# Performance work log

Measured on AMD Instinct MI355X. Metric: run time of the kernel, lower is better.

The kernel has to match this reference:

```python
import jax, jax.numpy as jnp
import numpy as np

H = 64  # GRU hidden size
EPS = 1e-6

def setup_inputs() -> dict:
    key = jax.random.key(0)
    ks = jax.random.split(key, 11)
    B, T = 1_000_000, 12
    return {
        "y_tm1": jax.random.normal(ks[0], (B, 2), jnp.float32),
        "z":     jax.random.normal(ks[1], (B, H), jnp.float32),
        "x":     jax.random.normal(ks[2], (B, T, 2), jnp.float32),  # base-dist sample, sigma=1.0
        "Wih":   jax.random.normal(ks[3], (3 * H, 2), jnp.float32) * 0.1,
        "Whh":   jax.random.normal(ks[4], (3 * H, H), jnp.float32) * 0.1,
        "bih":   jax.random.normal(ks[5], (3 * H,), jnp.float32) * 0.1,
        "bhh":   jax.random.normal(ks[6], (3 * H,), jnp.float32) * 0.1,
        "W1":    jax.random.normal(ks[7], (32, H), jnp.float32) * 0.1,
        "b1":    jax.random.normal(ks[8], (32,), jnp.float32) * 0.1,
        "W2":    jax.random.normal(ks[9], (4, 32), jnp.float32) * 0.1,
        "b2":    jax.random.normal(ks[10], (4,), jnp.float32) * 0.1,
    }

def _gru_cell(inp, h, Wih, Whh, bih, bhh):
    # torch.nn.GRUCell semantics; gates ordered (r, z, n)
    gi = inp @ Wih.T + bih              # [B, 3H]
    gh = h @ Whh.T + bhh                # [B, 3H]
    i_r, i_z, i_n = jnp.split(gi, 3, axis=-1)
    h_r, h_z, h_n = jnp.split(gh, 3, axis=-1)
    r = jax.nn.sigmoid(i_r + h_r)
    u = jax.nn.sigmoid(i_z + h_z)
    n = jnp.tanh(i_n + r * h_n)
    return (1.0 - u) * n + u * h

def reference(y_tm1, z, x, Wih, Whh, bih, bhh, W1, b1, W2, b2):
    def step(carry, x_t):
        y_prev, h = carry
        h = _gru_cell(y_prev, h, Wih, Whh, bih, bhh)
        dls = jax.nn.relu(h @ W1.T + b1) @ W2.T + b2   # [B, 4]
        dloc = dls[:, :2]
        scale = jax.nn.softplus(dls[:, 2:]) + EPS
        y_t = y_prev + dloc + scale * x_t
        return (y_t, h), y_t

    xs = jnp.swapaxes(x, 0, 1)                          # [T, B, 2]
    _, ys = jax.lax.scan(step, (y_tm1, z), xs)
    return jnp.swapaxes(ys, 0, 1)                       # [B, T, 2]
```

## Files before the change

kernel.cpp:

```cpp
#include <hip/hip_runtime.h>
#include <math.h>
#include <stdint.h>


typedef short bf16x8 __attribute__((ext_vector_type(8)));
typedef float f32x4  __attribute__((ext_vector_type(4)));

#define OFF_RZN 0
#define OFF_KS2 12288
#define OFF_W2F 14336
#define OFF_W1P 14848
#define WS_TOT  17152

#define W1LDW 72
#define HLW   104
#define XYW   28

__device__ __forceinline__ short f2bf(float f) {
    union { float f; uint32_t u; } v; v.f = f;
    uint32_t r = v.u + 0x7fffu + ((v.u >> 16) & 1u);
    return (short)(r >> 16);
}
__device__ __forceinline__ uint32_t cvtpk(float lo, float hi) {
    uint32_t r;
    asm("v_cvt_pk_bf16_f32 %0, %1, %2" : "=v"(r) : "v"(lo), "v"(hi));
    return r;
}
__device__ __forceinline__ float sigf(float x) {
    return __builtin_amdgcn_rcpf(1.f + __expf(-x));
}
__device__ __forceinline__ float tanhf1(float x) {
    return 1.f - 2.f * __builtin_amdgcn_rcpf(__expf(2.f * x) + 1.f);
}
__device__ __forceinline__ float softplusf(float x) {
    return fmaxf(x, 0.f) + __logf(1.f + __expf(-fabsf(x)));
}

__global__ void prep_kernel(const float* __restrict__ Wih, const float* __restrict__ Whh,
                            const float* __restrict__ bih, const float* __restrict__ bhh,
                            const float* __restrict__ W1, const float* __restrict__ W2,
                            short* __restrict__ wsw) {
    int idx = blockIdx.x * blockDim.x + threadIdx.x;
    if (idx >= WS_TOT) return;
    float v = 0.f;
    if (idx < OFF_KS2) {
        v = Whh[idx];
    } else if (idx < OFF_W2F) {
        int i = idx - OFF_KS2;
        int s = i >> 9, r = (i >> 3) & 63, j = i & 7;
        if (s == 0) {
            if (j == 0) v = Wih[2 * r];
            else if (j == 1) v = Wih[2 * r + 1];
            else if (j == 2) v = bih[r] + bhh[r];
        } else if (s == 1) {
            int row = 64 + r;
            if (j == 0) v = Wih[2 * row];
            else if (j == 1) v = Wih[2 * row + 1];
            else if (j == 2) v = bih[row] + bhh[row];
        } else if (s == 2) {
            if (j == 2) v = bhh[128 + r];
        } else {
            int row = 128 + r;
            if (j == 0) v = Wih[2 * row];
            else if (j == 1) v = Wih[2 * row + 1];
            else if (j == 2) v = bih[row];
        }
    } else if (idx < OFF_W1P) {
        int i = idx - OFF_W2F;
        int l = i >> 3, j = i & 7;
        int lnn = l & 15, gg = l >> 4;
        v = (lnn < 4) ? W2[lnn * 32 + gg * 8 + j] : 0.f;
    } else {
        int i = idx - OFF_W1P;
        int r = i / W1LDW, c = i - r * W1LDW;
        v = (c < 64) ? W1[r * 64 + c] : 0.f;
    }
    wsw[idx] = f2bf(v);
}

__global__ __launch_bounds__(256, 2)
void arflow4(const float* __restrict__ y_tm1,
             const float* __restrict__ z,
             const float* __restrict__ x,
             const float* __restrict__ b1,
             const float* __restrict__ b2,
             const short* __restrict__ wsw,
             float* __restrict__ out,
             int B, int T)
{
    __shared__ __align__(16) float XY[128 * XYW];
    __shared__ __align__(16) short HL[4][32 * HLW];
    __shared__ __align__(16) short KS2[4 * 64 * 8];
    __shared__ __align__(16) short W1L[32 * W1LDW];

    const int tid  = threadIdx.x;
    const int wave = tid >> 6;
    const int lane = tid & 63;
    const int g    = lane >> 4;
    const int ln   = lane & 15;
    const int base = blockIdx.x * 128;
    const int rows = (B - base < 128) ? (B - base) : 128;
    const int NF4  = T >> 1;
    const bool g0  = (g == 0);

    {
        const float4* xg = reinterpret_cast<const float4*>(x) + (size_t)base * NF4;
        const int tot = 128 * NF4;
        for (int i = tid; i < tot; i += 256) {
            float4 v = (i < rows * NF4) ? xg[i] : make_float4(0.f, 0.f, 0.f, 0.f);
            int r = i / NF4, c = i - r * NF4;
            *reinterpret_cast<float4*>(&XY[r * XYW + c * 4]) = v;
        }
    }
    {
        const uint32_t* src = reinterpret_cast<const uint32_t*>(wsw + OFF_KS2);
        uint32_t* dst = reinterpret_cast<uint32_t*>(KS2);
        for (int i = tid; i < 1024; i += 256) dst[i] = src[i];
        const uint32_t* s1 = reinterpret_cast<const uint32_t*>(wsw + OFF_W1P);
        uint32_t* d1 = reinterpret_cast<uint32_t*>(W1L);
        for (int i = tid; i < (32 * W1LDW) / 2; i += 256) d1[i] = s1[i];
    }

    bf16x8 wR[4][2], wZ[4][2], wN[4][2];
#pragma unroll
    for (int mg = 0; mg < 4; ++mg)
#pragma unroll
        for (int ks = 0; ks < 2; ++ks) {
            wR[mg][ks] = *reinterpret_cast<const bf16x8*>(wsw + ((      mg * 16 + ln) * 64 + ks * 32 + g * 8));
            wZ[mg][ks] = *reinterpret_cast<const bf16x8*>(wsw + ((64  + mg * 16 + ln) * 64 + ks * 32 + g * 8));
            wN[mg][ks] = *reinterpret_cast<const bf16x8*>(wsw + ((128 + mg * 16 + ln) * 64 + ks * 32 + g * 8));
        }
    bf16x8 w2f = *reinterpret_cast<const bf16x8*>(wsw + OFF_W2F + lane * 8);

    f32x4 b1q[2];
#pragma unroll
    for (int mt = 0; mt < 2; ++mt) {
        float4 tv = reinterpret_cast<const float4*>(b1)[mt * 4 + g];
        b1q[mt][0] = tv.x; b1q[mt][1] = tv.y; b1q[mt][2] = tv.z; b1q[mt][3] = tv.w;
    }
    f32x4 dInit;
    {
        float4 bb = *reinterpret_cast<const float4*>(b2);
        dInit[0] = g0 ? bb.x : 0.f;
        dInit[1] = g0 ? bb.y : 0.f;
        dInit[2] = g0 ? bb.z : 0.f;
        dInit[3] = g0 ? bb.w : 0.f;
    }
    const f32x4 Z0 = {0.f, 0.f, 0.f, 0.f};

    float hpr[4][2][4];
    float2 y[2];
    short* hl = &HL[wave][0];
#pragma unroll
    for (int n = 0; n < 2; ++n) {
        int gr = base + wave * 32 + n * 16 + ln;
        bool ok = gr < B;
#pragma unroll
        for (int mg = 0; mg < 4; ++mg) {
            float4 zv = ok ? reinterpret_cast<const float4*>(z)[(size_t)gr * 16 + mg * 4 + g]
                           : make_float4(0.f, 0.f, 0.f, 0.f);
            hpr[mg][n][0] = zv.x; hpr[mg][n][1] = zv.y;
            hpr[mg][n][2] = zv.z; hpr[mg][n][3] = zv.w;
        }
        float2 yv = ok ? reinterpret_cast<const float2*>(y_tm1)[gr] : make_float2(0.f, 0.f);
        y[n] = yv;
    }
#pragma unroll
    for (int n = 0; n < 2; ++n)
#pragma unroll
        for (int mg = 0; mg < 4; ++mg) {
            uint2 pk;
            pk.x = cvtpk(hpr[mg][n][0], hpr[mg][n][1]);
            pk.y = cvtpk(hpr[mg][n][2], hpr[mg][n][3]);
            *reinterpret_cast<uint2*>(&hl[(n * 16 + ln) * HLW + mg * 16 + g * 4]) = pk;
        }
    bf16x8 hb[2][2];
#pragma unroll
    for (int n = 0; n < 2; ++n)
#pragma unroll
        for (int ks = 0; ks < 2; ++ks)
            hb[n][ks] = *reinterpret_cast<const bf16x8*>(&hl[(n * 16 + ln) * HLW + ks * 32 + g * 8]);

    __syncthreads();

    const uint32_t onepk = g0 ? 0x00003F80u : 0u;
    const volatile bf16x8* k2p = reinterpret_cast<const volatile bf16x8*>(&KS2[ln * 8]);
    const volatile bf16x8* w1p = reinterpret_cast<const volatile bf16x8*>(&W1L[ln * W1LDW + g * 8]);

    for (int t = 0; t < T; ++t) {
        bf16x8 yb[2];
#pragma unroll
        for (int n = 0; n < 2; ++n) {
            uint32_t ypk = cvtpk(y[n].x, y[n].y);
            union { bf16x8 v; uint32_t u[4]; } yu;
            yu.u[0] = g0 ? ypk : 0u;
            yu.u[1] = onepk;
            yu.u[2] = 0u; yu.u[3] = 0u;
            yb[n] = yu.v;
        }

#pragma unroll
        for (int mg = 0; mg < 4; ++mg) {
            bf16x8 k2R = k2p[0 * 64 + mg * 16 + 0];
            bf16x8 k2Z = k2p[1 * 64 + mg * 16 + 0];
            bf16x8 k2N = k2p[2 * 64 + mg * 16 + 0];
            bf16x8 k2I = k2p[3 * 64 + mg * 16 + 0];
#pragma unroll
            for (int n = 0; n < 2; ++n) {
                f32x4 aR = __builtin_amdgcn_mfma_f32_16x16x32_bf16(wR[mg][0], hb[n][0], Z0, 0, 0, 0);
                f32x4 aZ = __builtin_amdgcn_mfma_f32_16x16x32_bf16(wZ[mg][0], hb[n][0], Z0, 0, 0, 0);
                f32x4 aN = __builtin_amdgcn_mfma_f32_16x16x32_bf16(wN[mg][0], hb[n][0], Z0, 0, 0, 0);
                f32x4 aI = __builtin_amdgcn_mfma_f32_16x16x32_bf16(k2I,       yb[n],    Z0, 0, 0, 0);
                aR = __builtin_amdgcn_mfma_f32_16x16x32_bf16(wR[mg][1], hb[n][1], aR, 0, 0, 0);
                aZ = __builtin_amdgcn_mfma_f32_16x16x32_bf16(wZ[mg][1], hb[n][1], aZ, 0, 0, 0);
                aN = __builtin_amdgcn_mfma_f32_16x16x32_bf16(wN[mg][1], hb[n][1], aN, 0, 0, 0);
                aR = __builtin_amdgcn_mfma_f32_16x16x32_bf16(k2R, yb[n], aR, 0, 0, 0);
                aZ = __builtin_amdgcn_mfma_f32_16x16x32_bf16(k2Z, yb[n], aZ, 0, 0, 0);
                aN = __builtin_amdgcn_mfma_f32_16x16x32_bf16(k2N, yb[n], aN, 0, 0, 0);

                float hq[4];
#pragma unroll
                for (int q = 0; q < 4; ++q) {
                    float r  = sigf(aR[q]);
                    float u  = sigf(aZ[q]);
                    float nn = tanhf1(fmaf(r, aN[q], aI[q]));
                    float hv = fmaf(u, hpr[mg][n][q] - nn, nn);
                    hpr[mg][n][q] = hv;
                    hq[q] = hv;
                }
                uint2 pk;
                pk.x = cvtpk(hq[0], hq[1]);
                pk.y = cvtpk(hq[2], hq[3]);
                *reinterpret_cast<uint2*>(&hl[(n * 16 + ln) * HLW + mg * 16 + g * 4]) = pk;
            }
        }

#pragma unroll
        for (int n = 0; n < 2; ++n)
#pragma unroll
            for (int ks = 0; ks < 2; ++ks)
                hb[n][ks] = *reinterpret_cast<const bf16x8*>(&hl[(n * 16 + ln) * HLW + ks * 32 + g * 8]);

        f32x4 aM[2][2];
#pragma unroll
        for (int mt = 0; mt < 2; ++mt) {
            bf16x8 wM0 = w1p[mt * 16 * (W1LDW / 8) + 0];
            bf16x8 wM1 = w1p[mt * 16 * (W1LDW / 8) + 4];
#pragma unroll
            for (int n = 0; n < 2; ++n) {
                f32x4 a = __builtin_amdgcn_mfma_f32_16x16x32_bf16(wM0, hb[n][0], b1q[mt], 0, 0, 0);
                aM[mt][n] = __builtin_amdgcn_mfma_f32_16x16x32_bf16(wM1, hb[n][1], a, 0, 0, 0);
            }
        }

#pragma unroll
        for (int n = 0; n < 2; ++n)
#pragma unroll
            for (int mt = 0; mt < 2; ++mt) {
                uint2 pk;
                pk.x = cvtpk(fmaxf(aM[mt][n][0], 0.f), fmaxf(aM[mt][n][1], 0.f));
                pk.y = cvtpk(fmaxf(aM[mt][n][2], 0.f), fmaxf(aM[mt][n][3], 0.f));
                *reinterpret_cast<uint2*>(&hl[(n * 16 + ln) * HLW + 64 + mt * 16 + g * 4]) = pk;
            }
        f32x4 aD[2];
#pragma unroll
        for (int n = 0; n < 2; ++n) {
            bf16x8 ab = *reinterpret_cast<const bf16x8*>(&hl[(n * 16 + ln) * HLW + 64 + g * 8]);
            aD[n] = __builtin_amdgcn_mfma_f32_16x16x32_bf16(w2f, ab, dInit, 0, 0, 0);
        }

#pragma unroll
        for (int n = 0; n < 2; ++n) {
            int rl = wave * 32 + n * 16 + ln;
            float2 xt = *reinterpret_cast<const float2*>(&XY[rl * XYW + t * 2]);
            float s0 = softplusf(aD[n][2]) + 1e-6f;
            float s1 = softplusf(aD[n][3]) + 1e-6f;
            y[n].x += aD[n][0] + s0 * xt.x;
            y[n].y += aD[n][1] + s1 * xt.y;
            if (g0)
                *reinterpret_cast<float2*>(&XY[rl * XYW + t * 2]) = y[n];
        }
    }

    __syncthreads();
    {
        float4* og = reinterpret_cast<float4*>(out) + (size_t)base * NF4;
        const int tot = 128 * NF4;
        for (int i = tid; i < tot; i += 256) {
            if (i < rows * NF4) {
                int r = i / NF4, c = i - r * NF4;
                og[i] = *reinterpret_cast<const float4*>(&XY[r * XYW + c * 4]);
            }
        }
    }
}

extern "C" void kernel_launch(void* const* d_in, const int* in_sizes, int n_in,
                              void* d_out, int out_size, void* d_ws, size_t ws_size,
                              hipStream_t stream) {
    const float* y_tm1 = (const float*)d_in[0];
    const float* z     = (const float*)d_in[1];
    const float* x     = (const float*)d_in[2];
    const float* Wih   = (const float*)d_in[3];
    const float* Whh   = (const float*)d_in[4];
    const float* bih   = (const float*)d_in[5];
    const float* bhh   = (const float*)d_in[6];
    const float* W1    = (const float*)d_in[7];
    const float* b1    = (const float*)d_in[8];
    const float* W2    = (const float*)d_in[9];
    const float* b2    = (const float*)d_in[10];
    float* out = (float*)d_out;
    short* wsw = (short*)d_ws;

    const int B = in_sizes[0] / 2;
    const int T = in_sizes[2] / in_sizes[0];

    hipLaunchKernelGGL(prep_kernel, dim3((WS_TOT + 255) / 256), dim3(256), 0, stream,
                       Wih, Whh, bih, bhh, W1, W2, wsw);

    const int nblk = (B + 127) / 128;
    hipLaunchKernelGGL(arflow4, dim3(nblk), dim3(256), 0, stream,
                       y_tm1, z, x, b1, b2, wsw, out, B, T);
}
```

Measured before the change: 908.3 us.

## Stream Whh fragments from global per step, fold exp scales into weights, raise occupancy

```diff
diff --git a/kernel.cpp b/kernel.cpp
--- a/kernel.cpp
+++ b/kernel.cpp
@@ -16,6 +16,9 @@
 #define HLW   104
 #define XYW   28
 
+#define SCL_RZ (-1.4426950408889634f)
+#define SCL_NI ( 2.8853900817779268f)
+
 __device__ __forceinline__ short f2bf(float f) {
     union { float f; uint32_t u; } v; v.f = f;
     uint32_t r = v.u + 0x7fffu + ((v.u >> 16) & 1u);
@@ -26,12 +29,7 @@
     asm("v_cvt_pk_bf16_f32 %0, %1, %2" : "=v"(r) : "v"(lo), "v"(hi));
     return r;
 }
-__device__ __forceinline__ float sigf(float x) {
-    return __builtin_amdgcn_rcpf(1.f + __expf(-x));
-}
-__device__ __forceinline__ float tanhf1(float x) {
-    return 1.f - 2.f * __builtin_amdgcn_rcpf(__expf(2.f * x) + 1.f);
-}
+__device__ __forceinline__ float rcpf(float x) { return __builtin_amdgcn_rcpf(x); }
 __device__ __forceinline__ float softplusf(float x) {
     return fmaxf(x, 0.f) + __logf(1.f + __expf(-fabsf(x)));
 }
@@ -44,10 +42,13 @@
     if (idx >= WS_TOT) return;
     float v = 0.f;
     if (idx < OFF_KS2) {
-        v = Whh[idx];
+        int row = idx >> 6;
+        float s = (row < 128) ? SCL_RZ : SCL_NI;
+        v = Whh[idx] * s;
     } else if (idx < OFF_W2F) {
         int i = idx - OFF_KS2;
         int s = i >> 9, r = (i >> 3) & 63, j = i & 7;
+        float sc = (s < 2) ? SCL_RZ : SCL_NI;
         if (s == 0) {
             if (j == 0) v = Wih[2 * r];
             else if (j == 1) v = Wih[2 * r + 1];
@@ -65,6 +66,7 @@
             else if (j == 1) v = Wih[2 * row + 1];
             else if (j == 2) v = bih[row];
         }
+        v *= sc;
     } else if (idx < OFF_W1P) {
         int i = idx - OFF_W2F;
         int l = i >> 3, j = i & 7;
@@ -78,8 +80,8 @@
     wsw[idx] = f2bf(v);
 }
 
-__global__ __launch_bounds__(256, 2)
-void arflow4(const float* __restrict__ y_tm1,
+__global__ __launch_bounds__(256, 3)
+void arflow5(const float* __restrict__ y_tm1,
              const float* __restrict__ z,
              const float* __restrict__ x,
              const float* __restrict__ b1,
@@ -121,15 +123,6 @@
         for (int i = tid; i < (32 * W1LDW) / 2; i += 256) d1[i] = s1[i];
     }
 
-    bf16x8 wR[4][2], wZ[4][2], wN[4][2];
-#pragma unroll
-    for (int mg = 0; mg < 4; ++mg)
-#pragma unroll
-        for (int ks = 0; ks < 2; ++ks) {
-            wR[mg][ks] = *reinterpret_cast<const bf16x8*>(wsw + ((      mg * 16 + ln) * 64 + ks * 32 + g * 8));
-            wZ[mg][ks] = *reinterpret_cast<const bf16x8*>(wsw + ((64  + mg * 16 + ln) * 64 + ks * 32 + g * 8));
-            wN[mg][ks] = *reinterpret_cast<const bf16x8*>(wsw + ((128 + mg * 16 + ln) * 64 + ks * 32 + g * 8));
-        }
     bf16x8 w2f = *reinterpret_cast<const bf16x8*>(wsw + OFF_W2F + lane * 8);
 
     f32x4 b1q[2];
@@ -138,14 +131,7 @@
         float4 tv = reinterpret_cast<const float4*>(b1)[mt * 4 + g];
         b1q[mt][0] = tv.x; b1q[mt][1] = tv.y; b1q[mt][2] = tv.z; b1q[mt][3] = tv.w;
     }
-    f32x4 dInit;
-    {
-        float4 bb = *reinterpret_cast<const float4*>(b2);
-        dInit[0] = g0 ? bb.x : 0.f;
-        dInit[1] = g0 ? bb.y : 0.f;
-        dInit[2] = g0 ? bb.z : 0.f;
-        dInit[3] = g0 ? bb.w : 0.f;
-    }
+    const float b20 = b2[0], b21 = b2[1], b22 = b2[2], b23 = b2[3];
     const f32x4 Z0 = {0.f, 0.f, 0.f, 0.f};
 
     float hpr[4][2][4];
@@ -187,7 +173,12 @@
     const volatile bf16x8* k2p = reinterpret_cast<const volatile bf16x8*>(&KS2[ln * 8]);
     const volatile bf16x8* w1p = reinterpret_cast<const volatile bf16x8*>(&W1L[ln * W1LDW + g * 8]);
 
+    const short* wp = wsw;
+    const int woff = ln * 8 + g;
+
     for (int t = 0; t < T; ++t) {
+        asm volatile("" : "+s"(wp));
+
         bf16x8 yb[2];
 #pragma unroll
         for (int n = 0; n < 2; ++n) {
@@ -201,19 +192,27 @@
 
 #pragma unroll
         for (int mg = 0; mg < 4; ++mg) {
-            bf16x8 k2R = k2p[0 * 64 + mg * 16 + 0];
-            bf16x8 k2Z = k2p[1 * 64 + mg * 16 + 0];
-            bf16x8 k2N = k2p[2 * 64 + mg * 16 + 0];
-            bf16x8 k2I = k2p[3 * 64 + mg * 16 + 0];
+            asm volatile("" : "+s"(wp));
+            const bf16x8* wq = reinterpret_cast<const bf16x8*>(wp) + woff;
+            bf16x8 wR0 = wq[(0 * 64 + mg * 16) * 8 + 0];
+            bf16x8 wR1 = wq[(0 * 64 + mg * 16) * 8 + 4];
+            bf16x8 wZ0 = wq[(1 * 64 + mg * 16) * 8 + 0];
+            bf16x8 wZ1 = wq[(1 * 64 + mg * 16) * 8 + 4];
+            bf16x8 wN0 = wq[(2 * 64 + mg * 16) * 8 + 0];
+            bf16x8 wN1 = wq[(2 * 64 + mg * 16) * 8 + 4];
+            bf16x8 k2R = k2p[0 * 64 + mg * 16];
+            bf16x8 k2Z = k2p[1 * 64 + mg * 16];
+            bf16x8 k2N = k2p[2 * 64 + mg * 16];
+            bf16x8 k2I = k2p[3 * 64 + mg * 16];
 #pragma unroll
             for (int n = 0; n < 2; ++n) {
-                f32x4 aR = __builtin_amdgcn_mfma_f32_16x16x32_bf16(wR[mg][0], hb[n][0], Z0, 0, 0, 0);
-                f32x4 aZ = __builtin_amdgcn_mfma_f32_16x16x32_bf16(wZ[mg][0], hb[n][0], Z0, 0, 0, 0);
-                f32x4 aN = __builtin_amdgcn_mfma_f32_16x16x32_bf16(wN[mg][0], hb[n][0], Z0, 0, 0, 0);
-                f32x4 aI = __builtin_amdgcn_mfma_f32_16x16x32_bf16(k2I,       yb[n],    Z0, 0, 0, 0);
-                aR = __builtin_amdgcn_mfma_f32_16x16x32_bf16(wR[mg][1], hb[n][1], aR, 0, 0, 0);
-                aZ = __builtin_amdgcn_mfma_f32_16x16x32_bf16(wZ[mg][1], hb[n][1], aZ, 0, 0, 0);
-                aN = __builtin_amdgcn_mfma_f32_16x16x32_bf16(wN[mg][1], hb[n][1], aN, 0, 0, 0);
+                f32x4 aR = __builtin_amdgcn_mfma_f32_16x16x32_bf16(wR0, hb[n][0], Z0, 0, 0, 0);
+                f32x4 aZ = __builtin_amdgcn_mfma_f32_16x16x32_bf16(wZ0, hb[n][0], Z0, 0, 0, 0);
+                f32x4 aN = __builtin_amdgcn_mfma_f32_16x16x32_bf16(wN0, hb[n][0], Z0, 0, 0, 0);
+                f32x4 aI = __builtin_amdgcn_mfma_f32_16x16x32_bf16(k2I, yb[n],    Z0, 0, 0, 0);
+                aR = __builtin_amdgcn_mfma_f32_16x16x32_bf16(wR1, hb[n][1], aR, 0, 0, 0);
+                aZ = __builtin_amdgcn_mfma_f32_16x16x32_bf16(wZ1, hb[n][1], aZ, 0, 0, 0);
+                aN = __builtin_amdgcn_mfma_f32_16x16x32_bf16(wN1, hb[n][1], aN, 0, 0, 0);
                 aR = __builtin_amdgcn_mfma_f32_16x16x32_bf16(k2R, yb[n], aR, 0, 0, 0);
                 aZ = __builtin_amdgcn_mfma_f32_16x16x32_bf16(k2Z, yb[n], aZ, 0, 0, 0);
                 aN = __builtin_amdgcn_mfma_f32_16x16x32_bf16(k2N, yb[n], aN, 0, 0, 0);
@@ -221,9 +220,10 @@
                 float hq[4];
 #pragma unroll
                 for (int q = 0; q < 4; ++q) {
-                    float r  = sigf(aR[q]);
-                    float u  = sigf(aZ[q]);
-                    float nn = tanhf1(fmaf(r, aN[q], aI[q]));
+                    float r  = rcpf(1.f + exp2f(aR[q]));
+                    float u  = rcpf(1.f + exp2f(aZ[q]));
+                    float ee = exp2f(fmaf(r, aN[q], aI[q]));
+                    float nn = fmaf(-2.f, rcpf(ee + 1.f), 1.f);
                     float hv = fmaf(u, hpr[mg][n][q] - nn, nn);
                     hpr[mg][n][q] = hv;
                     hq[q] = hv;
@@ -266,17 +266,17 @@
 #pragma unroll
         for (int n = 0; n < 2; ++n) {
             bf16x8 ab = *reinterpret_cast<const bf16x8*>(&hl[(n * 16 + ln) * HLW + 64 + g * 8]);
-            aD[n] = __builtin_amdgcn_mfma_f32_16x16x32_bf16(w2f, ab, dInit, 0, 0, 0);
+            aD[n] = __builtin_amdgcn_mfma_f32_16x16x32_bf16(w2f, ab, Z0, 0, 0, 0);
         }
 
 #pragma unroll
         for (int n = 0; n < 2; ++n) {
             int rl = wave * 32 + n * 16 + ln;
             float2 xt = *reinterpret_cast<const float2*>(&XY[rl * XYW + t * 2]);
-            float s0 = softplusf(aD[n][2]) + 1e-6f;
-            float s1 = softplusf(aD[n][3]) + 1e-6f;
-            y[n].x += aD[n][0] + s0 * xt.x;
-            y[n].y += aD[n][1] + s1 * xt.y;
+            float s0 = softplusf(aD[n][2] + b22) + 1e-6f;
+            float s1 = softplusf(aD[n][3] + b23) + 1e-6f;
+            y[n].x += (aD[n][0] + b20) + s0 * xt.x;
+            y[n].y += (aD[n][1] + b21) + s1 * xt.y;
             if (g0)
                 *reinterpret_cast<float2*>(&XY[rl * XYW + t * 2]) = y[n];
         }
@@ -319,6 +319,6 @@
                        Wih, Whh, bih, bhh, W1, W2, wsw);
 
     const int nblk = (B + 127) / 128;
-    hipLaunchKernelGGL(arflow4, dim3(nblk), dim3(256), 0, stream,
+    hipLaunchKernelGGL(arflow5, dim3(nblk), dim3(256), 0, stream,
                        y_tm1, z, x, b1, b2, wsw, out, B, T);
 }
```

After: 1.418 ms. 56.1% more time.
